# Kernel optimization log

Hardware: AMD Instinct MI355X
Metric: run time of the kernel (lower is better)

Reference implementation:

```python
import jax, jax.numpy as jnp
import numpy as np

# Static problem constants (must match setup_inputs)
NUM_GRAPHS = 64      # batch_size = int(batch[-1]) + 1
PTS_PER_GRAPH = 512
RATIO = 16           # centroids per graph
HEADS = 4
IN_CH = 64           # = out_channels per head (concat=False -> mean over heads)
NEG_SLOPE = 0.2


def setup_inputs() -> dict:
    key = jax.random.key(0)
    ks = jax.random.split(key, 8)
    N = NUM_GRAPHS * PTS_PER_GRAPH
    x = jax.random.normal(ks[0], (N, IN_CH), dtype=jnp.float32)
    edge_index = jnp.zeros((2, 2), dtype=jnp.int64)  # unused by forward
    batch = (jnp.arange(N) // PTS_PER_GRAPH).astype(jnp.int64)
    xcent_base = jax.random.normal(ks[1], (RATIO, IN_CH), dtype=jnp.float32)
    W_l = jax.random.normal(ks[2], (IN_CH, HEADS * IN_CH), dtype=jnp.float32) / np.sqrt(IN_CH)
    b_l = jax.random.normal(ks[3], (HEADS * IN_CH,), dtype=jnp.float32) * 0.01
    W_r = jax.random.normal(ks[4], (IN_CH, HEADS * IN_CH), dtype=jnp.float32) / np.sqrt(IN_CH)
    b_r = jax.random.normal(ks[5], (HEADS * IN_CH,), dtype=jnp.float32) * 0.01
    att = jax.random.normal(ks[6], (HEADS, IN_CH), dtype=jnp.float32) / np.sqrt(IN_CH)
    bias = jax.random.normal(ks[7], (IN_CH,), dtype=jnp.float32) * 0.01
    return {"x": x, "edge_index": edge_index, "batch": batch,
            "xcent_base": xcent_base, "W_l": W_l, "b_l": b_l,
            "W_r": W_r, "b_r": b_r, "att": att, "bias": bias}


def _bipart_pool(x, batch, xcent_base, W_l, b_l, W_r, b_r, att, bias):
    N = x.shape[0]
    B = NUM_GRAPHS
    Nc = B * RATIO  # number of centroid (target) nodes

    # Dense bipartite edges: each source node -> all RATIO centroids of its graph.
    src = jnp.repeat(jnp.arange(N, dtype=jnp.int32), RATIO)                     # [E]
    dst = jnp.tile(jnp.arange(RATIO, dtype=jnp.int32), N) \
        + jnp.repeat(batch.astype(jnp.int32), RATIO) * RATIO                    # [E]

    # PyG GATv2Conv(add_self_loops=True): remove src==dst edges, then add
    # self loops (i,i) for i < min(N_src, N_dst) = Nc. Keep static shapes by
    # masking the removed edges instead of deleting them.
    self_idx = jnp.arange(Nc, dtype=jnp.int32)
    src_f = jnp.concatenate([src, self_idx])
    dst_f = jnp.concatenate([dst, self_idx])
    drop = jnp.concatenate([src == dst, jnp.zeros((Nc,), dtype=bool)])          # [E+Nc]

    # Linear projections (source and target sides)
    x_l = (x @ W_l + b_l).reshape(N, HEADS, IN_CH)                              # [N,H,C]
    xcent = jnp.tile(xcent_base, (B, 1))                                        # [Nc,IN]
    x_r = (xcent @ W_r + b_r).reshape(Nc, HEADS, IN_CH)                         # [Nc,H,C]

    # GATv2 attention: leaky_relu(x_i + x_j) . att, softmax per target node
    xj = x_l[src_f]                                                             # [E',H,C]
    g = jax.nn.leaky_relu(xj + x_r[dst_f], NEG_SLOPE)
    alpha = jnp.einsum('ehc,hc->eh', g, att)                                    # [E',H]
    alpha = jnp.where(drop[:, None], jnp.float32(-1e30), alpha)
    amax = jax.ops.segment_max(alpha, dst_f, num_segments=Nc)                   # [Nc,H]
    e = jnp.exp(alpha - amax[dst_f])
    den = jax.ops.segment_sum(e, dst_f, num_segments=Nc)                        # [Nc,H]
    w = e / den[dst_f]                                                          # [E',H]

    out = jax.ops.segment_sum(w[..., None] * xj, dst_f, num_segments=Nc)        # [Nc,H,C]
    out = out.mean(axis=1) + bias                                               # concat=False -> mean heads
    return out.reshape(B, RATIO, IN_CH)


def reference(x, edge_index, batch, xcent_base, W_l, b_l, W_r, b_r, att, bias):
    xcent = _bipart_pool(x, batch, xcent_base, W_l, b_l, W_r, b_r, att, bias)
    batchcent = jnp.repeat(jnp.arange(NUM_GRAPHS, dtype=jnp.int64), RATIO)
    return xcent, batchcent
```

## Files before the change

### kernel.cpp

```cpp
#include <hip/hip_runtime.h>

#define PTS 512
#define CH  64
#define NC  1024

using s8v = __attribute__((ext_vector_type(8))) short;
using f4v = __attribute__((ext_vector_type(4))) float;

static __device__ __forceinline__ unsigned short f2b(float f) {
    unsigned u = __float_as_uint(f);
    return (unsigned short)((u + 0x7FFFu + ((u >> 16) & 1u)) >> 16);
}
static __device__ __forceinline__ float b2f(unsigned short s) {
    return __uint_as_float((unsigned)s << 16);
}

__global__ __launch_bounds__(256) void k0(
    const float* __restrict__ xcb, const float* __restrict__ W_r,
    const float* __restrict__ b_r, const float* __restrict__ att,
    const float* __restrict__ W_l,
    float* __restrict__ xr_ws, float* __restrict__ sxr_ws,
    unsigned short* __restrict__ Wt)
{
    __shared__ float s_row[256];
    const int blk = blockIdx.x, tid = threadIdx.x;
    if (blk < 16) {
        const int h = blk >> 2, rq = blk & 3;
        const int rl = tid >> 6, c = tid & 63;
        const int r = rq * 4 + rl;
        float acc = b_r[h * 64 + c];
        for (int k = 0; k < 64; ++k)
            acc = fmaf(xcb[r * 64 + k], W_r[k * 256 + h * 64 + c], acc);
        xr_ws[(h * 16 + r) * 64 + c] = acc;
        s_row[rl * 64 + c] = acc;
        __syncthreads();
        if (tid < 4) {
            float s = 0.f;
            for (int cc = 0; cc < 64; ++cc)
                s = fmaf(s_row[tid * 64 + cc], att[h * 64 + cc], s);
            sxr_ws[h * 16 + rq * 4 + tid] = s;
        }
    } else {
        int base = (blk - 16) * 2048;
        for (int t = tid; t < 2048; t += 256) {
            int idx = base + t;
            int h = idx >> 12, ch = (idx >> 6) & 63, k = idx & 63;
            Wt[idx] = f2b(W_l[k * 256 + h * 64 + ch]);
        }
    }
}

__global__ __launch_bounds__(256, 2) void k1(
    const float* __restrict__ x, const unsigned short* __restrict__ Wt,
    const float* __restrict__ b_l, const float* __restrict__ att,
    const float* __restrict__ xr_ws, const float* __restrict__ sxr_ws,
    const float* __restrict__ bias,
    float* __restrict__ aws, unsigned short* __restrict__ xlself,
    float* __restrict__ out)
{
    __shared__ unsigned short s_xl[64 * 264];

    const int tid = threadIdx.x;
    const int lane = tid & 63;
    const int w = __builtin_amdgcn_readfirstlane(tid >> 6);
    const int blk = blockIdx.x;
    const int row0 = blk * 64;
    const int l15 = lane & 15, quad = lane >> 4;

    f4v acc[4][4];
    const f4v zf = {0.f, 0.f, 0.f, 0.f};
#pragma unroll
    for (int m = 0; m < 4; ++m)
#pragma unroll
        for (int n = 0; n < 4; ++n) acc[m][n] = zf;

#pragma unroll
    for (int ks = 0; ks < 2; ++ks) {
        s8v Af[4], Bf[4];
#pragma unroll
        for (int m = 0; m < 4; ++m) {
            const float* xp = x + (size_t)(row0 + m * 16 + l15) * 64 + ks * 32 + quad * 8;
            float4 u0 = *(const float4*)xp;
            float4 u1 = *(const float4*)(xp + 4);
            s8v a;
            a[0] = (short)f2b(u0.x); a[1] = (short)f2b(u0.y);
            a[2] = (short)f2b(u0.z); a[3] = (short)f2b(u0.w);
            a[4] = (short)f2b(u1.x); a[5] = (short)f2b(u1.y);
            a[6] = (short)f2b(u1.z); a[7] = (short)f2b(u1.w);
            Af[m] = a;
        }
#pragma unroll
        for (int n = 0; n < 4; ++n)
            Bf[n] = *(const s8v*)(Wt + (size_t)(w * 64 + n * 16 + l15) * 64
                                  + ks * 32 + quad * 8);
#pragma unroll
        for (int m = 0; m < 4; ++m)
#pragma unroll
            for (int n = 0; n < 4; ++n)
                acc[m][n] = __builtin_amdgcn_mfma_f32_16x16x32_bf16(
                    Af[m], Bf[n], acc[m][n], 0, 0, 0);
    }

    float blv[4];
#pragma unroll
    for (int n = 0; n < 4; ++n) blv[n] = b_l[w * 64 + n * 16 + l15];
#pragma unroll
    for (int m = 0; m < 4; ++m)
#pragma unroll
        for (int n = 0; n < 4; ++n) {
            int ch = w * 64 + n * 16 + l15;
#pragma unroll
            for (int qq = 0; qq < 4; ++qq) {
                int row = m * 16 + quad * 4 + qq;
                s_xl[row * 264 + ch] = f2b(acc[m][n][qq] + blv[n]);
            }
        }

    if (blk >= 16 && blk < 20) {
        int base = (blk - 16) * 16384;
        float bv = bias[tid & 63];
#pragma unroll
        for (int j = 0; j < 64; ++j) out[base + j * 256 + tid] = bv;
    }
    if (blk == 20) {
#pragma unroll
        for (int j = 0; j < 4; ++j) {
            int c = j * 256 + tid;
            out[65536 + c] = (float)(c >> 4);
        }
    }

    __syncthreads();

    if (blk < 16) {
#pragma unroll
        for (int t = 0; t < 8; ++t) {
            int idx = tid + t * 256;
            int row = idx >> 5, co = (idx & 31) * 8;
            uint4 v = *(const uint4*)&s_xl[row * 264 + co];
            *(uint4*)&xlself[(size_t)(row0 + row) * 256 + co] = v;
        }
    }

    const float* attw = att + w * 64;
    const float* xrw  = xr_ws + w * 1024;
    float ac[16];
#pragma unroll
    for (int r = 0; r < 16; ++r) ac[r] = 0.f;
    float sxl = 0.f;

#pragma unroll
    for (int half = 0; half < 2; ++half) {
        const int cb = half * 32;
        float xlv[32], atv[32];
#pragma unroll
        for (int c8 = 0; c8 < 4; ++c8) {
            uint4 raw = *(const uint4*)&s_xl[lane * 264 + w * 64 + cb + c8 * 8];
            unsigned uu[4] = {raw.x, raw.y, raw.z, raw.w};
#pragma unroll
            for (int p = 0; p < 4; ++p) {
                xlv[c8 * 8 + 2 * p]     = __uint_as_float(uu[p] << 16);
                xlv[c8 * 8 + 2 * p + 1] = __uint_as_float(uu[p] & 0xffff0000u);
            }
        }
#pragma unroll
        for (int cq = 0; cq < 8; ++cq) {
            float4 a4 = *(const float4*)(attw + cb + cq * 4);
            atv[cq * 4 + 0] = a4.x; atv[cq * 4 + 1] = a4.y;
            atv[cq * 4 + 2] = a4.z; atv[cq * 4 + 3] = a4.w;
        }
#pragma unroll
        for (int t = 0; t < 32; ++t) sxl = fmaf(atv[t], xlv[t], sxl);

#pragma unroll 2
        for (int r = 0; r < 16; ++r) {
            const float4* xrp = (const float4*)(xrw + r * 64 + cb);
            float a = 0.f;
#pragma unroll
            for (int cq = 0; cq < 8; ++cq) {
                float4 x4 = xrp[cq];
                a = fmaf(atv[cq * 4 + 0], fabsf(xlv[cq * 4 + 0] + x4.x), a);
                a = fmaf(atv[cq * 4 + 1], fabsf(xlv[cq * 4 + 1] + x4.y), a);
                a = fmaf(atv[cq * 4 + 2], fabsf(xlv[cq * 4 + 2] + x4.z), a);
                a = fmaf(atv[cq * 4 + 3], fabsf(xlv[cq * 4 + 3] + x4.w), a);
            }
            ac[r] += a;
        }
    }

    float* ap = aws + ((size_t)(blk >> 3) * 4 + w) * 8192 + (blk & 7) * 64 + lane;
#pragma unroll
    for (int r = 0; r < 16; ++r)
        ap[r * 512] = 0.6f * (sxl + sxr_ws[w * 16 + r]) + 0.4f * ac[r];
}

__global__ __launch_bounds__(256, 4) void k2(
    const float* __restrict__ x, const float* __restrict__ W_l,
    const float* __restrict__ b_l, const float* __restrict__ aws,
    const unsigned short* __restrict__ xlself, float* __restrict__ out)
{
    __shared__ float s_et[2048];
    __shared__ float s_p[3072];
    __shared__ float sW[4096];
    __shared__ float s_f[16];

    const int q = blockIdx.x & 3, h = (blockIdx.x >> 2) & 3, b = blockIdx.x >> 4;
    const int tid = threadIdx.x;
    const float* abh = aws + (size_t)(b * 4 + h) * 8192;

    for (int idx = tid; idx < 4096; idx += 256)
        sW[idx] = W_l[(idx >> 6) * 256 + h * 64 + (idx & 63)];

    {
        const int r = tid >> 4, lg = tid & 15;
        const int snode = b * 16 + r;
        const float a_self = aws[(size_t)((snode >> 9) * 4 + h) * 8192
                                 + r * 512 + (snode & 511)];
        float m = a_self;
        for (int j = 0; j < 32; ++j) {
            int i = lg + j * 16;
            float a = abh[r * 512 + i];
            if (b == 0 && i == r) a = -1e30f;
            m = fmaxf(m, a);
        }
#pragma unroll
        for (int off = 8; off >= 1; off >>= 1) m = fmaxf(m, __shfl_xor(m, off));
        float d = 0.f;
        for (int j = 0; j < 32; ++j) {
            int i = lg + j * 16;
            float a = abh[r * 512 + i];
            d += (b == 0 && i == r) ? 0.f : __expf(a - m);
        }
#pragma unroll
        for (int off = 8; off >= 1; off >>= 1) d += __shfl_xor(d, off);
        const float es = __expf(a_self - m);
        const float inv = 1.f / (d + es);
        if (lg == 0) s_f[r] = es * inv;

        for (int j = 0; j < 8; ++j) {
            int iloc = lg + j * 16;
            int i = q * 128 + iloc;
            float a = abh[r * 512 + i];
            bool drop = (b == 0) && (i == r);
            s_et[iloc * 16 + r] = drop ? 0.f : __expf(a - m) * inv;
        }
    }
    __syncthreads();

    const int kt = tid & 15, rt = (tid >> 4) & 3, is = tid >> 6;
    float y4[4][4];
#pragma unroll
    for (int i = 0; i < 4; ++i)
#pragma unroll
        for (int j = 0; j < 4; ++j) y4[i][j] = 0.f;

    const float* xbq = x + ((size_t)b * PTS + q * 128 + is * 32) * 64;
#pragma unroll 4
    for (int i = 0; i < 32; ++i) {
        float4 xv = *(const float4*)(xbq + i * 64 + kt * 4);
        float4 ev = *(const float4*)&s_et[(is * 32 + i) * 16 + rt * 4];
        y4[0][0] = fmaf(ev.x, xv.x, y4[0][0]); y4[0][1] = fmaf(ev.x, xv.y, y4[0][1]);
        y4[0][2] = fmaf(ev.x, xv.z, y4[0][2]); y4[0][3] = fmaf(ev.x, xv.w, y4[0][3]);
        y4[1][0] = fmaf(ev.y, xv.x, y4[1][0]); y4[1][1] = fmaf(ev.y, xv.y, y4[1][1]);
        y4[1][2] = fmaf(ev.y, xv.z, y4[1][2]); y4[1][3] = fmaf(ev.y, xv.w, y4[1][3]);
        y4[2][0] = fmaf(ev.z, xv.x, y4[2][0]); y4[2][1] = fmaf(ev.z, xv.y, y4[2][1]);
        y4[2][2] = fmaf(ev.z, xv.z, y4[2][2]); y4[2][3] = fmaf(ev.z, xv.w, y4[2][3]);
        y4[3][0] = fmaf(ev.w, xv.x, y4[3][0]); y4[3][1] = fmaf(ev.w, xv.y, y4[3][1]);
        y4[3][2] = fmaf(ev.w, xv.z, y4[3][2]); y4[3][3] = fmaf(ev.w, xv.w, y4[3][3]);
    }

    if (is > 0) {
#pragma unroll
        for (int rr = 0; rr < 4; ++rr)
            *(float4*)&s_p[((is - 1) * 64 + rt * 16 + kt) * 16 + rr * 4] =
                make_float4(y4[rr][0], y4[rr][1], y4[rr][2], y4[rr][3]);
    }
    __syncthreads();
    float* s_yq = s_et;
    if (is == 0) {
#pragma unroll
        for (int j = 0; j < 3; ++j)
#pragma unroll
            for (int rr = 0; rr < 4; ++rr) {
                float4 v = *(const float4*)&s_p[(j * 64 + rt * 16 + kt) * 16 + rr * 4];
                y4[rr][0] += v.x; y4[rr][1] += v.y; y4[rr][2] += v.z; y4[rr][3] += v.w;
            }
#pragma unroll
        for (int rr = 0; rr < 4; ++rr)
            *(float4*)&s_yq[(rt * 4 + rr) * 64 + kt * 4] =
                make_float4(y4[rr][0], y4[rr][1], y4[rr][2], y4[rr][3]);
    }
    __syncthreads();

    {
        const int r2 = tid >> 4, ch = (tid & 15) * 4;
        float o0 = 0.f, o1 = 0.f, o2 = 0.f, o3 = 0.f;
#pragma unroll
        for (int k = 0; k < 64; ++k) {
            float yv = s_yq[r2 * 64 + k];
            float4 wv = *(const float4*)&sW[k * 64 + ch];
            o0 = fmaf(yv, wv.x, o0); o1 = fmaf(yv, wv.y, o1);
            o2 = fmaf(yv, wv.z, o2); o3 = fmaf(yv, wv.w, o3);
        }
        if (q == 0) {
            const float f = s_f[r2];
            const float* blp = b_l + h * 64 + ch;
            const unsigned short* xsp =
                xlself + (size_t)(b * 16 + r2) * 256 + h * 64 + ch;
            o0 += (1.f - f) * blp[0] + f * b2f(xsp[0]);
            o1 += (1.f - f) * blp[1] + f * b2f(xsp[1]);
            o2 += (1.f - f) * blp[2] + f * b2f(xsp[2]);
            o3 += (1.f - f) * blp[3] + f * b2f(xsp[3]);
        }
        float* op = out + (b * 16 + r2) * 64 + ch;
        atomicAdd(op + 0, 0.25f * o0); atomicAdd(op + 1, 0.25f * o1);
        atomicAdd(op + 2, 0.25f * o2); atomicAdd(op + 3, 0.25f * o3);
    }
}

extern "C" void kernel_launch(void* const* d_in, const int* in_sizes, int n_in,
                              void* d_out, int out_size, void* d_ws, size_t ws_size,
                              hipStream_t stream) {
    (void)in_sizes; (void)n_in; (void)out_size; (void)ws_size;
    const float* x    = (const float*)d_in[0];
    const float* xcb  = (const float*)d_in[3];
    const float* W_l  = (const float*)d_in[4];
    const float* b_l  = (const float*)d_in[5];
    const float* W_r  = (const float*)d_in[6];
    const float* b_r  = (const float*)d_in[7];
    const float* att  = (const float*)d_in[8];
    const float* bias = (const float*)d_in[9];
    float* out = (float*)d_out;

    float* wsf = (float*)d_ws;
    float*          aws    = wsf;
    float*          xr_ws  = wsf + 2097152;
    float*          sxr_ws = wsf + 2101248;
    unsigned short* Wt     = (unsigned short*)(wsf + 2101376);
    unsigned short* xlself = (unsigned short*)(wsf + 2109568);

    hipLaunchKernelGGL(k0, dim3(24), dim3(256), 0, stream,
                       xcb, W_r, b_r, att, W_l, xr_ws, sxr_ws, Wt);
    hipLaunchKernelGGL(k1, dim3(512), dim3(256), 0, stream,
                       x, Wt, b_l, att, xr_ws, sxr_ws, bias, aws, xlself, out);
    hipLaunchKernelGGL(k2, dim3(1024), dim3(256), 0, stream,
                       x, W_l, b_l, aws, xlself, out);
}
```

Baseline: 133.8 us.

## Split softmax stats and W_l projection out of aggregation kernel

Softmax max/denominator statistics are computed once per (graph, head) in a new kernel instead of being recomputed by each of the four quarter-blocks. The aggregation kernel now only builds normalized weights and partial sums into a workspace, and a separate kernel sums the partials and applies the W_l projection once per (graph, head). This removes repeated reads of the attention row and repeated W_l loads per quarter, and cuts atomics by four times. Bias initialization moves into k0. The cost is two extra launches and a round-trip of partial results through global memory.

```diff
diff --git a/kernel.cpp b/kernel.cpp
--- a/kernel.cpp
+++ b/kernel.cpp
@@ -18,9 +18,9 @@
 __global__ __launch_bounds__(256) void k0(
     const float* __restrict__ xcb, const float* __restrict__ W_r,
     const float* __restrict__ b_r, const float* __restrict__ att,
-    const float* __restrict__ W_l,
+    const float* __restrict__ W_l, const float* __restrict__ bias,
     float* __restrict__ xr_ws, float* __restrict__ sxr_ws,
-    unsigned short* __restrict__ Wt)
+    unsigned short* __restrict__ Wt, float* __restrict__ out)
 {
     __shared__ float s_row[256];
     const int blk = blockIdx.x, tid = threadIdx.x;
@@ -40,13 +40,25 @@
                 s = fmaf(s_row[tid * 64 + cc], att[h * 64 + cc], s);
             sxr_ws[h * 16 + rq * 4 + tid] = s;
         }
-    } else {
+    } else if (blk < 24) {
         int base = (blk - 16) * 2048;
         for (int t = tid; t < 2048; t += 256) {
             int idx = base + t;
             int h = idx >> 12, ch = (idx >> 6) & 63, k = idx & 63;
             Wt[idx] = f2b(W_l[k * 256 + h * 64 + ch]);
         }
+    } else {
+        int base = (blk - 24) * 16384;
+        float bv = bias[tid & 63];
+#pragma unroll
+        for (int j = 0; j < 64; ++j) out[base + j * 256 + tid] = bv;
+        if (blk == 27) {
+#pragma unroll
+            for (int j = 0; j < 4; ++j) {
+                int c = j * 256 + tid;
+                out[65536 + c] = (float)(c >> 4);
+            }
+        }
     }
 }
 
@@ -54,9 +66,7 @@
     const float* __restrict__ x, const unsigned short* __restrict__ Wt,
     const float* __restrict__ b_l, const float* __restrict__ att,
     const float* __restrict__ xr_ws, const float* __restrict__ sxr_ws,
-    const float* __restrict__ bias,
-    float* __restrict__ aws, unsigned short* __restrict__ xlself,
-    float* __restrict__ out)
+    float* __restrict__ aws, unsigned short* __restrict__ xlself)
 {
     __shared__ unsigned short s_xl[64 * 264];
 
@@ -115,21 +125,6 @@
                 s_xl[row * 264 + ch] = f2b(acc[m][n][qq] + blv[n]);
             }
         }
-
-    if (blk >= 16 && blk < 20) {
-        int base = (blk - 16) * 16384;
-        float bv = bias[tid & 63];
-#pragma unroll
-        for (int j = 0; j < 64; ++j) out[base + j * 256 + tid] = bv;
-    }
-    if (blk == 20) {
-#pragma unroll
-        for (int j = 0; j < 4; ++j) {
-            int c = j * 256 + tid;
-            out[65536 + c] = (float)(c >> 4);
-        }
-    }
-
     __syncthreads();
 
     if (blk < 16) {
@@ -194,56 +189,65 @@
         ap[r * 512] = 0.6f * (sxl + sxr_ws[w * 16 + r]) + 0.4f * ac[r];
 }
 
-__global__ __launch_bounds__(256, 4) void k2(
-    const float* __restrict__ x, const float* __restrict__ W_l,
-    const float* __restrict__ b_l, const float* __restrict__ aws,
-    const unsigned short* __restrict__ xlself, float* __restrict__ out)
-{
-    __shared__ float s_et[2048];
+__global__ __launch_bounds__(256) void k1c(
+    const float* __restrict__ aws, float* __restrict__ m_arr,
+    float* __restrict__ inv_arr, float* __restrict__ f_arr)
+{
+    const int bh = blockIdx.x, b = bh >> 2, h = bh & 3;
+    const int tid = threadIdx.x;
+    const int r = tid >> 4, lg = tid & 15;
+    const float* ar = aws + (size_t)bh * 8192 + r * 512;
+    const int snode = b * 16 + r;
+    const float a_self = aws[(size_t)((snode >> 9) * 4 + h) * 8192
+                             + r * 512 + (snode & 511)];
+    float m = a_self;
+    for (int j = 0; j < 32; ++j) {
+        int i = lg + j * 16;
+        float a = ar[i];
+        if (b == 0 && i == r) a = -1e30f;
+        m = fmaxf(m, a);
+    }
+#pragma unroll
+    for (int off = 8; off >= 1; off >>= 1) m = fmaxf(m, __shfl_xor(m, off));
+    float d = 0.f;
+    for (int j = 0; j < 32; ++j) {
+        int i = lg + j * 16;
+        float a = ar[i];
+        d += (b == 0 && i == r) ? 0.f : __expf(a - m);
+    }
+#pragma unroll
+    for (int off = 8; off >= 1; off >>= 1) d += __shfl_xor(d, off);
+    if (lg == 0) {
+        float es = __expf(a_self - m);
+        float inv = 1.f / (d + es);
+        m_arr[bh * 16 + r] = m;
+        inv_arr[bh * 16 + r] = inv;
+        f_arr[bh * 16 + r] = es * inv;
+    }
+}
+
+__global__ __launch_bounds__(256, 4) void k2agg(
+    const float* __restrict__ x, const float* __restrict__ aws,
+    const float* __restrict__ m_arr, const float* __restrict__ inv_arr,
+    float* __restrict__ yws)
+{
+    __shared__ float s_et[2560];
     __shared__ float s_p[3072];
-    __shared__ float sW[4096];
-    __shared__ float s_f[16];
+    __shared__ float s_m[16], s_inv[16];
 
     const int q = blockIdx.x & 3, h = (blockIdx.x >> 2) & 3, b = blockIdx.x >> 4;
+    const int bh = b * 4 + h;
     const int tid = threadIdx.x;
-    const float* abh = aws + (size_t)(b * 4 + h) * 8192;
-
-    for (int idx = tid; idx < 4096; idx += 256)
-        sW[idx] = W_l[(idx >> 6) * 256 + h * 64 + (idx & 63)];
-
-    {
-        const int r = tid >> 4, lg = tid & 15;
-        const int snode = b * 16 + r;
-        const float a_self = aws[(size_t)((snode >> 9) * 4 + h) * 8192
-                                 + r * 512 + (snode & 511)];
-        float m = a_self;
-        for (int j = 0; j < 32; ++j) {
-            int i = lg + j * 16;
-            float a = abh[r * 512 + i];
-            if (b == 0 && i == r) a = -1e30f;
-            m = fmaxf(m, a);
-        }
-#pragma unroll
-        for (int off = 8; off >= 1; off >>= 1) m = fmaxf(m, __shfl_xor(m, off));
-        float d = 0.f;
-        for (int j = 0; j < 32; ++j) {
-            int i = lg + j * 16;
-            float a = abh[r * 512 + i];
-            d += (b == 0 && i == r) ? 0.f : __expf(a - m);
-        }
-#pragma unroll
-        for (int off = 8; off >= 1; off >>= 1) d += __shfl_xor(d, off);
-        const float es = __expf(a_self - m);
-        const float inv = 1.f / (d + es);
-        if (lg == 0) s_f[r] = es * inv;
-
-        for (int j = 0; j < 8; ++j) {
-            int iloc = lg + j * 16;
-            int i = q * 128 + iloc;
-            float a = abh[r * 512 + i];
-            bool drop = (b == 0) && (i == r);
-            s_et[iloc * 16 + r] = drop ? 0.f : __expf(a - m) * inv;
-        }
+
+    if (tid < 16) { s_m[tid] = m_arr[bh * 16 + tid]; s_inv[tid] = inv_arr[bh * 16 + tid]; }
+    __syncthreads();
+
+    for (int idx = tid; idx < 2048; idx += 256) {
+        int r = idx >> 7, i_loc = idx & 127;
+        int i = q * 128 + i_loc;
+        float a = aws[(size_t)bh * 8192 + r * 512 + i];
+        bool drop = (b == 0) && (i == r);
+        s_et[i_loc * 20 + r] = drop ? 0.f : __expf(a - s_m[r]) * s_inv[r];
     }
     __syncthreads();
 
@@ -258,7 +262,7 @@
 #pragma unroll 4
     for (int i = 0; i < 32; ++i) {
         float4 xv = *(const float4*)(xbq + i * 64 + kt * 4);
-        float4 ev = *(const float4*)&s_et[(is * 32 + i) * 16 + rt * 4];
+        float4 ev = *(const float4*)&s_et[(is * 32 + i) * 20 + rt * 4];
         y4[0][0] = fmaf(ev.x, xv.x, y4[0][0]); y4[0][1] = fmaf(ev.x, xv.y, y4[0][1]);
         y4[0][2] = fmaf(ev.x, xv.z, y4[0][2]); y4[0][3] = fmaf(ev.x, xv.w, y4[0][3]);
         y4[1][0] = fmaf(ev.y, xv.x, y4[1][0]); y4[1][1] = fmaf(ev.y, xv.y, y4[1][1]);
@@ -276,7 +280,6 @@
                 make_float4(y4[rr][0], y4[rr][1], y4[rr][2], y4[rr][3]);
     }
     __syncthreads();
-    float* s_yq = s_et;
     if (is == 0) {
 #pragma unroll
         for (int j = 0; j < 3; ++j)
@@ -285,37 +288,51 @@
                 float4 v = *(const float4*)&s_p[(j * 64 + rt * 16 + kt) * 16 + rr * 4];
                 y4[rr][0] += v.x; y4[rr][1] += v.y; y4[rr][2] += v.z; y4[rr][3] += v.w;
             }
+        float* yq = yws + (size_t)(bh * 4 + q) * 1024;
 #pragma unroll
         for (int rr = 0; rr < 4; ++rr)
-            *(float4*)&s_yq[(rt * 4 + rr) * 64 + kt * 4] =
+            *(float4*)&yq[(rt * 4 + rr) * 64 + kt * 4] =
                 make_float4(y4[rr][0], y4[rr][1], y4[rr][2], y4[rr][3]);
     }
-    __syncthreads();
-
-    {
-        const int r2 = tid >> 4, ch = (tid & 15) * 4;
-        float o0 = 0.f, o1 = 0.f, o2 = 0.f, o3 = 0.f;
-#pragma unroll
-        for (int k = 0; k < 64; ++k) {
-            float yv = s_yq[r2 * 64 + k];
-            float4 wv = *(const float4*)&sW[k * 64 + ch];
-            o0 = fmaf(yv, wv.x, o0); o1 = fmaf(yv, wv.y, o1);
-            o2 = fmaf(yv, wv.z, o2); o3 = fmaf(yv, wv.w, o3);
-        }
-        if (q == 0) {
-            const float f = s_f[r2];
-            const float* blp = b_l + h * 64 + ch;
-            const unsigned short* xsp =
-                xlself + (size_t)(b * 16 + r2) * 256 + h * 64 + ch;
-            o0 += (1.f - f) * blp[0] + f * b2f(xsp[0]);
-            o1 += (1.f - f) * blp[1] + f * b2f(xsp[1]);
-            o2 += (1.f - f) * blp[2] + f * b2f(xsp[2]);
-            o3 += (1.f - f) * blp[3] + f * b2f(xsp[3]);
-        }
-        float* op = out + (b * 16 + r2) * 64 + ch;
-        atomicAdd(op + 0, 0.25f * o0); atomicAdd(op + 1, 0.25f * o1);
-        atomicAdd(op + 2, 0.25f * o2); atomicAdd(op + 3, 0.25f * o3);
-    }
+}
+
+__global__ __launch_bounds__(256) void k3(
+    const float* __restrict__ yws, const float* __restrict__ W_l,
+    const float* __restrict__ b_l, const float* __restrict__ f_arr,
+    const unsigned short* __restrict__ xlself, float* __restrict__ out)
+{
+    __shared__ float s_y[1024];
+    __shared__ float sW[4096];
+
+    const int bh = blockIdx.x, b = bh >> 2, h = bh & 3;
+    const int tid = threadIdx.x;
+
+    const float* yq = yws + (size_t)bh * 4096;
+    for (int o = tid; o < 1024; o += 256)
+        s_y[o] = yq[o] + yq[1024 + o] + yq[2048 + o] + yq[3072 + o];
+    for (int idx = tid; idx < 4096; idx += 256)
+        sW[idx] = W_l[(idx >> 6) * 256 + h * 64 + (idx & 63)];
+    __syncthreads();
+
+    const int r2 = tid >> 4, ch = (tid & 15) * 4;
+    float o0 = 0.f, o1 = 0.f, o2 = 0.f, o3 = 0.f;
+#pragma unroll
+    for (int k = 0; k < 64; ++k) {
+        float yv = s_y[r2 * 64 + k];
+        float4 wv = *(const float4*)&sW[k * 64 + ch];
+        o0 = fmaf(yv, wv.x, o0); o1 = fmaf(yv, wv.y, o1);
+        o2 = fmaf(yv, wv.z, o2); o3 = fmaf(yv, wv.w, o3);
+    }
+    const float f = f_arr[bh * 16 + r2];
+    const float* blp = b_l + h * 64 + ch;
+    const unsigned short* xsp = xlself + (size_t)(b * 16 + r2) * 256 + h * 64 + ch;
+    o0 += (1.f - f) * blp[0] + f * b2f(xsp[0]);
+    o1 += (1.f - f) * blp[1] + f * b2f(xsp[1]);
+    o2 += (1.f - f) * blp[2] + f * b2f(xsp[2]);
+    o3 += (1.f - f) * blp[3] + f * b2f(xsp[3]);
+    float* op = out + (b * 16 + r2) * 64 + ch;
+    atomicAdd(op + 0, 0.25f * o0); atomicAdd(op + 1, 0.25f * o1);
+    atomicAdd(op + 2, 0.25f * o2); atomicAdd(op + 3, 0.25f * o3);
 }
 
 extern "C" void kernel_launch(void* const* d_in, const int* in_sizes, int n_in,
@@ -338,11 +355,19 @@
     float*          sxr_ws = wsf + 2101248;
     unsigned short* Wt     = (unsigned short*)(wsf + 2101376);
     unsigned short* xlself = (unsigned short*)(wsf + 2109568);
-
-    hipLaunchKernelGGL(k0, dim3(24), dim3(256), 0, stream,
-                       xcb, W_r, b_r, att, W_l, xr_ws, sxr_ws, Wt);
+    float*          m_arr  = wsf + 2240640;
+    float*          inv_a  = wsf + 2244736;
+    float*          f_arr  = wsf + 2248832;
+    float*          yws    = wsf + 2252928;
+
+    hipLaunchKernelGGL(k0, dim3(28), dim3(256), 0, stream,
+                       xcb, W_r, b_r, att, W_l, bias, xr_ws, sxr_ws, Wt, out);
     hipLaunchKernelGGL(k1, dim3(512), dim3(256), 0, stream,
-                       x, Wt, b_l, att, xr_ws, sxr_ws, bias, aws, xlself, out);
-    hipLaunchKernelGGL(k2, dim3(1024), dim3(256), 0, stream,
-                       x, W_l, b_l, aws, xlself, out);
-}
+                       x, Wt, b_l, att, xr_ws, sxr_ws, aws, xlself);
+    hipLaunchKernelGGL(k1c, dim3(256), dim3(256), 0, stream,
+                       aws, m_arr, inv_a, f_arr);
+    hipLaunchKernelGGL(k2agg, dim3(1024), dim3(256), 0, stream,
+                       x, aws, m_arr, inv_a, yws);
+    hipLaunchKernelGGL(k3, dim3(256), dim3(256), 0, stream,
+                       yws, W_l, b_l, f_arr, xlself, out);
+}
```

Result: faster. 130.7 us (-2.3%).
